# Performance work log

Hardware: AMD Instinct MI355X
Metric: run time of the kernel (lower is better)

## Reference

```python
import jax, jax.numpy as jnp
import numpy as np

B, Te, Td, D_ENC, D_DEC, ATT = 8, 512, 128, 512, 512, 256


def setup_inputs() -> dict:
    key = jax.random.key(0)
    k0, k1, k2, k3, k4 = jax.random.split(key, 5)
    return {
        "values": jax.random.normal(k0, (B, Te, D_ENC), dtype=jnp.float32),
        "query": jax.random.normal(k1, (B, Td, D_DEC), dtype=jnp.float32),
        "W_h": jax.random.uniform(k2, (D_ENC, ATT), jnp.float32, -0.05, 0.05),
        "U_a": jax.random.uniform(k3, (D_DEC, ATT), jnp.float32, -0.05, 0.05),
        "V_a": jax.random.uniform(k4, (1, ATT), jnp.float32, -0.05, 0.05),
    }


def reference(values, query, W_h, U_a, V_a):
    # values: [B, Te, D_ENC] encoder output sequence (single entry in 'values' list)
    # query:  [B, Td, D_DEC] decoder output sequence
    # With a single encoder sequence, broadcast_sum/broadcast_concat reduces are identities.
    W_hi = jnp.einsum('bse,ea->bsa', values, W_h)        # [B, Te, ATT]
    U_a_dot_s = jnp.einsum('btd,da->bta', query, U_a)    # [B, Td, ATT]
    # tanh(h.Wa + s.Ua): vectorized over all decoder timesteps (K.rnn scan unrolled)
    act = jnp.tanh(W_hi[:, None, :, :] + U_a_dot_s[:, :, None, :])  # [B, Td, Te, ATT]
    scores = jnp.einsum('btsa,a->bts', act, V_a[0])      # [B, Td, Te]
    e_outputs = jax.nn.softmax(scores, axis=-1)          # softmax over encoder positions
    # context: weighted sum of encoder hidden states
    c_outputs = jnp.einsum('bts,bse->bte', e_outputs, values)  # [B, Td, D_ENC]
    return (c_outputs, e_outputs)
```

## Files before the change

kernel.cpp:

```cpp
#include <hip/hip_runtime.h>
#include <hip/hip_bf16.h>


typedef __attribute__((ext_vector_type(8))) short bf16x8;
typedef __attribute__((ext_vector_type(4))) float f32x4;

__device__ inline void f32_to_bf16_pair(float x, short& h, short& l) {
    unsigned u = __builtin_bit_cast(unsigned, x);
    unsigned r = u + 0x7FFFu + ((u >> 16) & 1u);
    h = (short)(r >> 16);
    float xh = __builtin_bit_cast(float, r & 0xFFFF0000u);
    float xl = x - xh;
    unsigned u2 = __builtin_bit_cast(unsigned, xl);
    unsigned r2 = u2 + 0x7FFFu + ((u2 >> 16) & 1u);
    l = (short)(r2 >> 16);
}

__global__ __launch_bounds__(256) void prep(
    const float* __restrict__ W_h, const float* __restrict__ U_a,
    const float* __restrict__ values, const float* __restrict__ query,
    short* __restrict__ BHi, short* __restrict__ BLo,
    short* __restrict__ AHi, short* __restrict__ ALo)
{
    __shared__ float TW[64][65];
    __shared__ float TA[16][516];
    const int bid = blockIdx.x;
    const int tid = threadIdx.x;

    if (bid < 64) {
        const int mat = bid >> 5, nb = (bid >> 3) & 3, kb = bid & 7;
        const float* W = mat ? U_a : W_h;
        {
            const int krow = tid >> 2, cq = (tid & 3) * 16;
            const float* src = W + (size_t)(kb * 64 + krow) * 256 + nb * 64 + cq;
            #pragma unroll
            for (int q = 0; q < 4; ++q)
                *(float4*)&TW[krow][cq + q * 4] = *(const float4*)&src[q * 4];
        }
        __syncthreads();
        {
            const int f = tid >> 5;
            const int ngl = f >> 1, ksl = f & 1;
            const int l0 = (tid & 31) * 2;
            const int ngrp = nb * 4 + ngl;
            const int ksg = kb * 2 + ksl;
            const size_t base = (size_t)mat * 131072 + (size_t)(ngrp * 16 + ksg) * 512;
            #pragma unroll
            for (int li = 0; li < 2; ++li) {
                const int lane = l0 + li;
                const int lr = lane & 15, lg = lane >> 4;
                bf16x8 hv, lv;
                #pragma unroll
                for (int j = 0; j < 8; ++j) {
                    short h, l;
                    f32_to_bf16_pair(TW[ksl * 32 + lg * 8 + j][ngl * 16 + lr], h, l);
                    hv[j] = h; lv[j] = l;
                }
                *(bf16x8*)(BHi + base + lane * 8) = hv;
                *(bf16x8*)(BLo + base + lane * 8) = lv;
            }
        }
    } else {
        const int mg = bid - 64;
        const float* src = (mg < 256) ? values + (size_t)mg * 16 * 512
                                      : query + (size_t)(mg - 256) * 16 * 512;
        {
            const int row = tid >> 4, c0 = (tid & 15) * 4;
            #pragma unroll
            for (int i = 0; i < 8; ++i)
                *(float4*)&TA[row][c0 + i * 64] =
                    *(const float4*)&src[(size_t)row * 512 + c0 + i * 64];
        }
        __syncthreads();
        {
            const int ks = tid >> 4;
            const int l4 = (tid & 15) * 4;
            const size_t base = ((size_t)(mg * 16 + ks)) * 512;
            #pragma unroll
            for (int li = 0; li < 4; ++li) {
                const int lane = l4 + li;
                const int lr = lane & 15, lg = lane >> 4;
                bf16x8 hv, lv;
                #pragma unroll
                for (int j = 0; j < 8; ++j) {
                    short h, l;
                    f32_to_bf16_pair(TA[lr][ks * 32 + lg * 8 + j], h, l);
                    hv[j] = h; lv[j] = l;
                }
                *(bf16x8*)(AHi + base + lane * 8) = hv;
                *(bf16x8*)(ALo + base + lane * 8) = lv;
            }
        }
    }
}

__global__ __launch_bounds__(128) void gemm_mfma(
    const short* __restrict__ AHi, const short* __restrict__ ALo,
    const short* __restrict__ BHi, const short* __restrict__ BLo,
    float* __restrict__ EwO, float* __restrict__ EuO)
{
    const int bid = blockIdx.x;
    const int mt = bid >> 2, nt = bid & 3;
    const int tid = threadIdx.x;
    const int w = tid >> 6, l = tid & 63;
    const int lr = l & 15, lg = l >> 4;

    float* C; int m0, mg, matoff;
    if (mt < 128) { C = EwO; m0 = mt * 32; mg = mt * 2 + w; matoff = 0; }
    else { C = EuO; m0 = (mt - 128) * 32; mg = 256 + (mt - 128) * 2 + w; matoff = 131072; }

    const short* ah_p = AHi + ((size_t)mg * 16) * 512 + l * 8;
    const short* al_p = ALo + ((size_t)mg * 16) * 512 + l * 8;
    const short* bh_p = BHi + matoff + ((size_t)(nt * 4) * 16) * 512 + l * 8;
    const short* bl_p = BLo + matoff + ((size_t)(nt * 4) * 16) * 512 + l * 8;

    f32x4 acc[4];
    #pragma unroll
    for (int nc = 0; nc < 4; ++nc) acc[nc] = (f32x4){0.f, 0.f, 0.f, 0.f};

    #pragma unroll 2
    for (int ks = 0; ks < 16; ++ks) {
        bf16x8 ah = *(const bf16x8*)(ah_p + (size_t)ks * 512);
        bf16x8 al = *(const bf16x8*)(al_p + (size_t)ks * 512);
        #pragma unroll
        for (int nc = 0; nc < 4; ++nc) {
            bf16x8 bh = *(const bf16x8*)(bh_p + ((size_t)(nc * 16 + ks)) * 512);
            bf16x8 bl = *(const bf16x8*)(bl_p + ((size_t)(nc * 16 + ks)) * 512);
            acc[nc] = __builtin_amdgcn_mfma_f32_16x16x32_bf16(ah, bh, acc[nc], 0, 0, 0);
            acc[nc] = __builtin_amdgcn_mfma_f32_16x16x32_bf16(al, bh, acc[nc], 0, 0, 0);
            acc[nc] = __builtin_amdgcn_mfma_f32_16x16x32_bf16(ah, bl, acc[nc], 0, 0, 0);
        }
    }

    const float SCL = 2.8853900817779268f;
    float* cp = C + (size_t)(m0 + w * 16 + lg * 4) * 256 + nt * 64 + lr;
    #pragma unroll
    for (int nc = 0; nc < 4; ++nc)
        #pragma unroll
        for (int r = 0; r < 4; ++r)
            cp[(size_t)r * 256 + nc * 16] = __builtin_amdgcn_exp2f(acc[nc][r] * SCL);
}

__global__ __launch_bounds__(256) void scores_k(
    const float* __restrict__ Ew, const float* __restrict__ Eu,
    const float* __restrict__ Va, float* __restrict__ scoresP)
{
    __shared__ float Ws[64][68];
    __shared__ float Us[16][68];

    const int bid = blockIdx.x;
    const int b = bid & 7;
    const int rest = bid >> 3;
    const int ah = rest & 3;
    const int tt = (rest >> 2) & 7;
    const int st = rest >> 5;
    const int t0 = tt * 16, s0 = st * 64, a0 = ah * 64;
    const int tid = threadIdx.x;

    const int r = tid >> 2, c16 = (tid & 3) * 16;
    const float* wsrc = Ew + (size_t)(b * 512 + s0 + r) * 256 + a0 + c16;
    #pragma unroll
    for (int q = 0; q < 4; ++q)
        *(float4*)&Ws[r][c16 + q * 4] = *(const float4*)&wsrc[q * 4];
    const int r8 = tid >> 4, c8 = (tid & 15) * 4;
    const float* usrc = Eu + (size_t)(b * 128 + t0 + r8) * 256 + a0 + c8;
    *(float4*)&Us[r8][c8] = *(const float4*)&usrc[0];
    __syncthreads();

    const int t = tid >> 4;
    const int ss = tid & 15;
    const float* Vp = Va + a0;

    float acc[4] = {};
    #pragma unroll 4
    for (int a = 0; a < 64; a += 4) {
        float4 u  = *(const float4*)&Us[t][a];
        float4 w0 = *(const float4*)&Ws[ss][a];
        float4 w1 = *(const float4*)&Ws[ss + 16][a];
        float4 w2 = *(const float4*)&Ws[ss + 32][a];
        float4 w3 = *(const float4*)&Ws[ss + 48][a];
        const float uv[4] = {u.x, u.y, u.z, u.w};
        const float wv[4][4] = {{w0.x, w0.y, w0.z, w0.w}, {w1.x, w1.y, w1.z, w1.w},
                                {w2.x, w2.y, w2.z, w2.w}, {w3.x, w3.y, w3.z, w3.w}};
        #pragma unroll
        for (int q = 0; q < 4; ++q) {
            const float vq = Vp[a + q];
            #pragma unroll
            for (int k = 0; k < 4; ++k) {
                float rc = __builtin_amdgcn_rcpf(fmaf(wv[k][q], uv[q], 1.f));
                acc[k] = fmaf(vq, rc, acc[k]);
            }
        }
    }

    float* sp = scoresP + (size_t)ah * 524288
              + (size_t)(b * 128 + t0 + t) * 512 + s0 + ss;
    #pragma unroll
    for (int k = 0; k < 4; ++k) sp[k * 16] = acc[k];
}

__global__ __launch_bounds__(256) void softctx(
    const float* __restrict__ scoresP, const float* __restrict__ values,
    float* __restrict__ out_c, float* __restrict__ out_e)
{
    __shared__ float Ps[4][512];
    __shared__ float Part[7][4][128];

    const int bid = blockIdx.x;
    const int b = bid & 7;
    const int rest = bid >> 3;
    const int tg = rest & 31;
    const int eh = rest >> 5;
    const int t0 = tg * 4;
    const int tid = threadIdx.x;

    {
        const int row = tid >> 6, lane = tid & 63;
        const float* sp = scoresP + (size_t)(b * 128 + t0 + row) * 512;
        float e[8]; float ssum = 0.f;
        #pragma unroll
        for (int k = 0; k < 8; ++k) {
            const int idx = k * 64 + lane;
            float s = sp[idx] + sp[524288 + idx] + sp[1048576 + idx] + sp[1572864 + idx];
            e[k] = __builtin_amdgcn_exp2f(s * -2.8853900817779268f);
            ssum += e[k];
        }
        #pragma unroll
        for (int off = 32; off > 0; off >>= 1)
            ssum += __shfl_xor(ssum, off);
        const float inv = 1.0f / ssum;
        float* erow = out_e + (size_t)(b * 128 + t0 + row) * 512;
        #pragma unroll
        for (int k = 0; k < 8; ++k) {
            float p = e[k] * inv;
            Ps[row][k * 64 + lane] = p;
            if (eh == 0) erow[k * 64 + lane] = p;
        }
    }
    __syncthreads();

    const int sh = tid >> 5;
    const int el = (tid & 31) * 4;
    const int e4 = eh * 128 + el;
    const int sb = sh * 64;
    const float* vb = values + (size_t)b * 262144;

    float4 a0 = {0,0,0,0}, a1 = {0,0,0,0}, a2 = {0,0,0,0}, a3 = {0,0,0,0};
    #pragma unroll 2
    for (int s2 = 0; s2 < 64; s2 += 4) {
        float4 q0 = *(const float4*)&Ps[0][sb + s2];
        float4 q1 = *(const float4*)&Ps[1][sb + s2];
        float4 q2 = *(const float4*)&Ps[2][sb + s2];
        float4 q3 = *(const float4*)&Ps[3][sb + s2];
        const float q0v[4] = {q0.x, q0.y, q0.z, q0.w};
        const float q1v[4] = {q1.x, q1.y, q1.z, q1.w};
        const float q2v[4] = {q2.x, q2.y, q2.z, q2.w};
        const float q3v[4] = {q3.x, q3.y, q3.z, q3.w};
        #pragma unroll
        for (int j = 0; j < 4; ++j) {
            float4 v4 = *(const float4*)&vb[(size_t)(sb + s2 + j) * 512 + e4];
            a0.x = fmaf(q0v[j], v4.x, a0.x); a0.y = fmaf(q0v[j], v4.y, a0.y);
            a0.z = fmaf(q0v[j], v4.z, a0.z); a0.w = fmaf(q0v[j], v4.w, a0.w);
            a1.x = fmaf(q1v[j], v4.x, a1.x); a1.y = fmaf(q1v[j], v4.y, a1.y);
            a1.z = fmaf(q1v[j], v4.z, a1.z); a1.w = fmaf(q1v[j], v4.w, a1.w);
            a2.x = fmaf(q2v[j], v4.x, a2.x); a2.y = fmaf(q2v[j], v4.y, a2.y);
            a2.z = fmaf(q2v[j], v4.z, a2.z); a2.w = fmaf(q2v[j], v4.w, a2.w);
            a3.x = fmaf(q3v[j], v4.x, a3.x); a3.y = fmaf(q3v[j], v4.y, a3.y);
            a3.z = fmaf(q3v[j], v4.z, a3.z); a3.w = fmaf(q3v[j], v4.w, a3.w);
        }
    }

    if (sh) {
        *(float4*)&Part[sh - 1][0][el] = a0;
        *(float4*)&Part[sh - 1][1][el] = a1;
        *(float4*)&Part[sh - 1][2][el] = a2;
        *(float4*)&Part[sh - 1][3][el] = a3;
    }
    __syncthreads();
    if (!sh) {
        #pragma unroll
        for (int rrow = 0; rrow < 4; ++rrow) {
            float4 acc = (rrow == 0) ? a0 : (rrow == 1) ? a1 : (rrow == 2) ? a2 : a3;
            #pragma unroll
            for (int g = 0; g < 7; ++g) {
                float4 p4 = *(const float4*)&Part[g][rrow][el];
                acc.x += p4.x; acc.y += p4.y; acc.z += p4.z; acc.w += p4.w;
            }
            *(float4*)&out_c[(size_t)(b * 128 + t0 + rrow) * 512 + e4] = acc;
        }
    }
}

extern "C" void kernel_launch(void* const* d_in, const int* in_sizes, int n_in,
                              void* d_out, int out_size, void* d_ws, size_t ws_size,
                              hipStream_t stream) {
    const float* values = (const float*)d_in[0];
    const float* query  = (const float*)d_in[1];
    const float* W_h    = (const float*)d_in[2];
    const float* U_a    = (const float*)d_in[3];
    const float* V_a    = (const float*)d_in[4];

    float* ws      = (float*)d_ws;
    float* Ew      = ws;
    float* Eu      = ws + 1048576;
    float* scoresP = ws + 1310720;
    short* S       = (short*)(ws + 3407872);
    short* AHi     = S;
    short* ALo     = S + 2621440;
    short* BHi     = S + 5242880;
    short* BLo     = S + 5505024;

    float* out_c = (float*)d_out;
    float* out_e = out_c + 8 * 128 * 512;

    hipLaunchKernelGGL(prep, dim3(384), dim3(256), 0, stream,
                       W_h, U_a, values, query, BHi, BLo, AHi, ALo);
    hipLaunchKernelGGL(gemm_mfma, dim3(640), dim3(128), 0, stream,
                       AHi, ALo, BHi, BLo, Ew, Eu);
    hipLaunchKernelGGL(scores_k, dim3(2048), dim3(256), 0, stream,
                       Ew, Eu, V_a, scoresP);
    hipLaunchKernelGGL(softctx, dim3(1024), dim3(256), 0, stream,
                       scoresP, values, out_c, out_e);
}
```

Measured before the change: 56.09 us.

## Double per-thread tile rows in scores and softmax-context kernels

The scores kernel now has each thread compute two decoder rows (32 per block instead of 16), so every Ws tile loaded into shared memory is reused twice and the grid is halved. The softmax-context kernel handles 8 decoder rows per block instead of 4, so each float4 of values read from global memory feeds twice as many FMAs and the number of blocks reading values is halved. The cost is more registers and LDS per block and fewer blocks, which lowers parallelism and occupancy.

```diff
diff --git a/kernel.cpp b/kernel.cpp
--- a/kernel.cpp
+++ b/kernel.cpp
@@ -146,95 +146,104 @@
     const float* __restrict__ Va, float* __restrict__ scoresP)
 {
     __shared__ float Ws[64][68];
-    __shared__ float Us[16][68];
+    __shared__ float Us[32][68];
 
     const int bid = blockIdx.x;
     const int b = bid & 7;
     const int rest = bid >> 3;
     const int ah = rest & 3;
-    const int tt = (rest >> 2) & 7;
-    const int st = rest >> 5;
-    const int t0 = tt * 16, s0 = st * 64, a0 = ah * 64;
+    const int tt = (rest >> 2) & 3;
+    const int st = rest >> 4;
+    const int t0 = tt * 32, s0 = st * 64, a0 = ah * 64;
     const int tid = threadIdx.x;
 
-    const int r = tid >> 2, c16 = (tid & 3) * 16;
-    const float* wsrc = Ew + (size_t)(b * 512 + s0 + r) * 256 + a0 + c16;
-    #pragma unroll
-    for (int q = 0; q < 4; ++q)
-        *(float4*)&Ws[r][c16 + q * 4] = *(const float4*)&wsrc[q * 4];
-    const int r8 = tid >> 4, c8 = (tid & 15) * 4;
-    const float* usrc = Eu + (size_t)(b * 128 + t0 + r8) * 256 + a0 + c8;
-    *(float4*)&Us[r8][c8] = *(const float4*)&usrc[0];
+    {
+        const int r = tid >> 2, c16 = (tid & 3) * 16;
+        const float* wsrc = Ew + (size_t)(b * 512 + s0 + r) * 256 + a0 + c16;
+        #pragma unroll
+        for (int q = 0; q < 4; ++q)
+            *(float4*)&Ws[r][c16 + q * 4] = *(const float4*)&wsrc[q * 4];
+        const int r8 = tid >> 3, c8 = (tid & 7) * 8;
+        const float* usrc = Eu + (size_t)(b * 128 + t0 + r8) * 256 + a0 + c8;
+        *(float4*)&Us[r8][c8]     = *(const float4*)&usrc[0];
+        *(float4*)&Us[r8][c8 + 4] = *(const float4*)&usrc[4];
+    }
     __syncthreads();
 
-    const int t = tid >> 4;
+    const int tb = tid >> 4;
     const int ss = tid & 15;
     const float* Vp = Va + a0;
 
-    float acc[4] = {};
-    #pragma unroll 4
+    float acc[2][4] = {};
+    #pragma unroll 2
     for (int a = 0; a < 64; a += 4) {
-        float4 u  = *(const float4*)&Us[t][a];
+        float4 u0 = *(const float4*)&Us[tb][a];
+        float4 u1 = *(const float4*)&Us[tb + 16][a];
         float4 w0 = *(const float4*)&Ws[ss][a];
         float4 w1 = *(const float4*)&Ws[ss + 16][a];
         float4 w2 = *(const float4*)&Ws[ss + 32][a];
         float4 w3 = *(const float4*)&Ws[ss + 48][a];
-        const float uv[4] = {u.x, u.y, u.z, u.w};
+        const float uv[2][4] = {{u0.x, u0.y, u0.z, u0.w}, {u1.x, u1.y, u1.z, u1.w}};
         const float wv[4][4] = {{w0.x, w0.y, w0.z, w0.w}, {w1.x, w1.y, w1.z, w1.w},
                                 {w2.x, w2.y, w2.z, w2.w}, {w3.x, w3.y, w3.z, w3.w}};
         #pragma unroll
         for (int q = 0; q < 4; ++q) {
             const float vq = Vp[a + q];
             #pragma unroll
-            for (int k = 0; k < 4; ++k) {
-                float rc = __builtin_amdgcn_rcpf(fmaf(wv[k][q], uv[q], 1.f));
-                acc[k] = fmaf(vq, rc, acc[k]);
-            }
+            for (int i = 0; i < 2; ++i)
+                #pragma unroll
+                for (int k = 0; k < 4; ++k) {
+                    float rc = __builtin_amdgcn_rcpf(fmaf(wv[k][q], uv[i][q], 1.f));
+                    acc[i][k] = fmaf(vq, rc, acc[i][k]);
+                }
         }
     }
 
     float* sp = scoresP + (size_t)ah * 524288
-              + (size_t)(b * 128 + t0 + t) * 512 + s0 + ss;
-    #pragma unroll
-    for (int k = 0; k < 4; ++k) sp[k * 16] = acc[k];
+              + (size_t)(b * 128 + t0 + tb) * 512 + s0 + ss;
+    #pragma unroll
+    for (int k = 0; k < 4; ++k) sp[k * 16] = acc[0][k];
+    sp += (size_t)16 * 512;
+    #pragma unroll
+    for (int k = 0; k < 4; ++k) sp[k * 16] = acc[1][k];
 }
 
 __global__ __launch_bounds__(256) void softctx(
     const float* __restrict__ scoresP, const float* __restrict__ values,
     float* __restrict__ out_c, float* __restrict__ out_e)
 {
-    __shared__ float Ps[4][512];
-    __shared__ float Part[7][4][128];
+    __shared__ float Ps[8][512];
+    __shared__ float Part[7][8][128];
 
     const int bid = blockIdx.x;
     const int b = bid & 7;
     const int rest = bid >> 3;
-    const int tg = rest & 31;
-    const int eh = rest >> 5;
-    const int t0 = tg * 4;
+    const int tg = rest & 15;
+    const int eh = rest >> 4;
+    const int t0 = tg * 8;
     const int tid = threadIdx.x;
 
     {
-        const int row = tid >> 6, lane = tid & 63;
+        const int row = tid >> 5, lane = tid & 31;
         const float* sp = scoresP + (size_t)(b * 128 + t0 + row) * 512;
-        float e[8]; float ssum = 0.f;
-        #pragma unroll
-        for (int k = 0; k < 8; ++k) {
-            const int idx = k * 64 + lane;
+        float e[16]; float ssum = 0.f;
+        #pragma unroll
+        for (int k = 0; k < 16; ++k) {
+            const int idx = k * 32 + lane;
             float s = sp[idx] + sp[524288 + idx] + sp[1048576 + idx] + sp[1572864 + idx];
             e[k] = __builtin_amdgcn_exp2f(s * -2.8853900817779268f);
             ssum += e[k];
         }
         #pragma unroll
-        for (int off = 32; off > 0; off >>= 1)
+        for (int off = 16; off > 0; off >>= 1)
             ssum += __shfl_xor(ssum, off);
         const float inv = 1.0f / ssum;
         float* erow = out_e + (size_t)(b * 128 + t0 + row) * 512;
         #pragma unroll
-        for (int k = 0; k < 8; ++k) {
+        for (int k = 0; k < 16; ++k) {
             float p = e[k] * inv;
-            Ps[row][k * 64 + lane] = p;
-            if (eh == 0) erow[k * 64 + lane] = p;
+            Ps[row][k * 32 + lane] = p;
+            if (eh == 0) erow[k * 32 + lane] = p;
         }
     }
     __syncthreads();
@@ -245,48 +254,47 @@
     const int sb = sh * 64;
     const float* vb = values + (size_t)b * 262144;
 
-    float4 a0 = {0,0,0,0}, a1 = {0,0,0,0}, a2 = {0,0,0,0}, a3 = {0,0,0,0};
+    f32x4 a[8];
+    #pragma unroll
+    for (int r = 0; r < 8; ++r) a[r] = (f32x4){0.f, 0.f, 0.f, 0.f};
+
     #pragma unroll 2
     for (int s2 = 0; s2 < 64; s2 += 4) {
-        float4 q0 = *(const float4*)&Ps[0][sb + s2];
-        float4 q1 = *(const float4*)&Ps[1][sb + s2];
-        float4 q2 = *(const float4*)&Ps[2][sb + s2];
-        float4 q3 = *(const float4*)&Ps[3][sb + s2];
-        const float q0v[4] = {q0.x, q0.y, q0.z, q0.w};
-        const float q1v[4] = {q1.x, q1.y, q1.z, q1.w};
-        const float q2v[4] = {q2.x, q2.y, q2.z, q2.w};
-        const float q3v[4] = {q3.x, q3.y, q3.z, q3.w};
+        float4 q[8];
+        #pragma unroll
+        for (int r = 0; r < 8; ++r)
+            q[r] = *(const float4*)&Ps[r][sb + s2];
         #pragma unroll
         for (int j = 0; j < 4; ++j) {
             float4 v4 = *(const float4*)&vb[(size_t)(sb + s2 + j) * 512 + e4];
-            a0.x = fmaf(q0v[j], v4.x, a0.x); a0.y = fmaf(q0v[j], v4.y, a0.y);
-            a0.z = fmaf(q0v[j], v4.z, a0.z); a0.w = fmaf(q0v[j], v4.w, a0.w);
-            a1.x = fmaf(q1v[j], v4.x, a1.x); a1.y = fmaf(q1v[j], v4.y, a1.y);
-            a1.z = fmaf(q1v[j], v4.z, a1.z); a1.w = fmaf(q1v[j], v4.w, a1.w);
-            a2.x = fmaf(q2v[j], v4.x, a2.x); a2.y = fmaf(q2v[j], v4.y, a2.y);
-            a2.z = fmaf(q2v[j], v4.z, a2.z); a2.w = fmaf(q2v[j], v4.w, a2.w);
-            a3.x = fmaf(q3v[j], v4.x, a3.x); a3.y = fmaf(q3v[j], v4.y, a3.y);
-            a3.z = fmaf(q3v[j], v4.z, a3.z); a3.w = fmaf(q3v[j], v4.w, a3.w);
+            #pragma unroll
+            for (int r = 0; r < 8; ++r) {
+                const float qv = (j == 0) ? q[r].x : (j == 1) ? q[r].y
+                               : (j == 2) ? q[r].z : q[r].w;
+                a[r][0] = fmaf(qv, v4.x, a[r][0]);
+                a[r][1] = fmaf(qv, v4.y, a[r][1]);
+                a[r][2] = fmaf(qv, v4.z, a[r][2]);
+                a[r][3] = fmaf(qv, v4.w, a[r][3]);
+            }
         }
     }
 
     if (sh) {
-        *(float4*)&Part[sh - 1][0][el] = a0;
-        *(float4*)&Part[sh - 1][1][el] = a1;
-        *(float4*)&Part[sh - 1][2][el] = a2;
-        *(float4*)&Part[sh - 1][3][el] = a3;
+        #pragma unroll
+        for (int r = 0; r < 8; ++r)
+            *(f32x4*)&Part[sh - 1][r][el] = a[r];
     }
     __syncthreads();
     if (!sh) {
         #pragma unroll
-        for (int rrow = 0; rrow < 4; ++rrow) {
-            float4 acc = (rrow == 0) ? a0 : (rrow == 1) ? a1 : (rrow == 2) ? a2 : a3;
+        for (int r = 0; r < 8; ++r) {
+            f32x4 accv = a[r];
             #pragma unroll
             for (int g = 0; g < 7; ++g) {
-                float4 p4 = *(const float4*)&Part[g][rrow][el];
-                acc.x += p4.x; acc.y += p4.y; acc.z += p4.z; acc.w += p4.w;
+                float4 p4 = *(const float4*)&Part[g][r][el];
+                accv[0] += p4.x; accv[1] += p4.y; accv[2] += p4.z; accv[3] += p4.w;
             }
-            *(float4*)&out_c[(size_t)(b * 128 + t0 + rrow) * 512 + e4] = acc;
+            *(f32x4*)&out_c[(size_t)(b * 128 + t0 + r) * 512 + e4] = accv;
         }
     }
 }
@@ -317,8 +325,8 @@
                        W_h, U_a, values, query, BHi, BLo, AHi, ALo);
     hipLaunchKernelGGL(gemm_mfma, dim3(640), dim3(128), 0, stream,
                        AHi, ALo, BHi, BLo, Ew, Eu);
-    hipLaunchKernelGGL(scores_k, dim3(2048), dim3(256), 0, stream,
+    hipLaunchKernelGGL(scores_k, dim3(1024), dim3(256), 0, stream,
                        Ew, Eu, V_a, scoresP);
-    hipLaunchKernelGGL(softctx, dim3(1024), dim3(256), 0, stream,
+    hipLaunchKernelGGL(softctx, dim3(512), dim3(256), 0, stream,
                        scoresP, values, out_c, out_e);
 }
```

Measured after the change: 52.74 us, median of 2. 1.06x faster.
